# Kernel tuning notes

Measured on AMD Instinct MI355X. Metric: run time of the kernel, lower is better.

Reference implementation:

```python
import jax, jax.numpy as jnp
import numpy as np

N = 100000   # num nodes
E = 1600000  # num edges (before self-loops)
D_IN, D_HID, D_OUT = 128, 128, 64


def _gcn_layer(x, W, b, src, dst, norm):
    # GCNConv: h = x @ W, then normalized sparse aggregation, then bias.
    h = x @ W                              # [N, d_out]
    msg = h[src] * norm[:, None]           # [E+N, d_out] gathered + scaled messages
    out = jax.ops.segment_sum(msg, dst, num_segments=N)  # scatter-add to dst nodes
    return out + b


def reference(x, W1, b1, W2, b2, edge_index):
    src0, dst0 = edge_index[0], edge_index[1]
    # GCNConv adds self-loops by default
    loop = jnp.arange(N, dtype=src0.dtype)
    src = jnp.concatenate([src0, loop])
    dst = jnp.concatenate([dst0, loop])
    # symmetric normalization: deg^{-1/2}[src] * deg^{-1/2}[dst]
    deg = jax.ops.segment_sum(jnp.ones_like(src, dtype=x.dtype), dst, num_segments=N)
    dinv = jnp.where(deg > 0, jax.lax.rsqrt(jnp.maximum(deg, 1.0)), 0.0)
    norm = dinv[src] * dinv[dst]           # [E+N]

    h = jax.nn.relu(_gcn_layer(x, W1, b1, src, dst, norm))
    return _gcn_layer(h, W2, b2, src, dst, norm)


def setup_inputs() -> dict:
    key = jax.random.key(0)
    k1, k2, k3, k4 = jax.random.split(key, 4)
    x = jax.random.normal(k1, (N, D_IN), dtype=jnp.float32)
    # glorot-ish init for weights
    W1 = jax.random.normal(k2, (D_IN, D_HID), dtype=jnp.float32) * (1.0 / np.sqrt(D_IN))
    b1 = jnp.zeros((D_HID,), dtype=jnp.float32)
    W2 = jax.random.normal(k3, (D_HID, D_OUT), dtype=jnp.float32) * (1.0 / np.sqrt(D_HID))
    b2 = jnp.zeros((D_OUT,), dtype=jnp.float32)
    edge_index = jax.random.randint(k4, (2, E), 0, N, dtype=jnp.int64)
    return {"x": x, "W1": W1, "b1": b1, "W2": W2, "b2": b2, "edge_index": edge_index}
```

## Files before the change

kernel.cpp:

```cpp
#include <hip/hip_runtime.h>

static constexpr int NN = 100000;
static constexpr int EE = 1600000;
static constexpr int BSZ = 64;
static constexpr int NB = (NN + BSZ - 1) / BSZ;
static constexpr int BCAP = 2048;
static constexpr int TILE = 2048;
static constexpr int GB = 2048;


__device__ __forceinline__ unsigned short f2bf(float f) {
    unsigned u = __float_as_uint(f);
    u += 0x7FFFu + ((u >> 16) & 1u);
    return (unsigned short)(u >> 16);
}
__device__ __forceinline__ float bfl(unsigned u) { return __uint_as_float(u << 16); }
__device__ __forceinline__ float bfh(unsigned u) { return __uint_as_float(u & 0xFFFF0000u); }

typedef __attribute__((ext_vector_type(8))) short short8;
typedef __attribute__((ext_vector_type(4))) float float4v;


__global__ __launch_bounds__(256) void k_init(const float* __restrict__ W1,
                                              const float* __restrict__ W2,
                                              unsigned short* __restrict__ W1t,
                                              unsigned short* __restrict__ W2t,
                                              int* __restrict__ bcur) {
    int idx = blockIdx.x * 256 + threadIdx.x;
    if (idx < 16384) {
        int n = idx >> 7, k = idx & 127;
        W1t[idx] = f2bf(W1[k * 128 + n]);
    } else if (idx < 24576) {
        int j = idx - 16384;
        int n = j >> 7, k = j & 127;
        W2t[j] = f2bf(W2[k * 64 + n]);
    } else if (idx < 24576 + NB) {
        int b = idx - 24576;
        bcur[b] = b * BCAP;
    }
}


__global__ __launch_bounds__(256) void k_bin(const int* __restrict__ src,
                                             const int* __restrict__ dst,
                                             int* __restrict__ bcur,
                                             int* __restrict__ ebuf, int E) {
    constexpr int K = TILE / 256;
    __shared__ int lcnt[NB];
    __shared__ int lbase[NB];
    const int t = threadIdx.x;
    const int e0 = blockIdx.x * TILE;

    for (int i = t; i < NB; i += 256) lcnt[i] = 0;
    __syncthreads();

    int dreg[K], ofs[K];
#pragma unroll
    for (int k = 0; k < K; ++k) {
        int e = e0 + k * 256 + t;
        if (e < E) {
            int d = dst[e];
            dreg[k] = d;
            ofs[k] = atomicAdd(&lcnt[d >> 6], 1);
        } else dreg[k] = -1;
    }
    __syncthreads();

    for (int i = t; i < NB; i += 256) {
        int c = lcnt[i];
        lbase[i] = c ? atomicAdd(&bcur[i], c) : 0;
    }
    __syncthreads();

#pragma unroll
    for (int k = 0; k < K; ++k) {
        if (dreg[k] >= 0) {
            int e = e0 + k * 256 + t;
            int s = src[e];
            int b = dreg[k] >> 6;
            ebuf[lbase[b] + ofs[k]] = (s << 6) | (dreg[k] & 63);
        }
    }
}


__global__ __launch_bounds__(512) void k_bscan(const int* __restrict__ bcur,
                                               int* __restrict__ gbase) {
    const int t = threadIdx.x;
    const int lane = t & 63, wid = t >> 6;
    int v[4]; int s = 0;
#pragma unroll
    for (int k = 0; k < 4; ++k) {
        int b = t * 4 + k;
        v[k] = (b < NB) ? (bcur[b] - b * BCAP) : 0;
        s += v[k];
    }
    int x = s;
#pragma unroll
    for (int off = 1; off < 64; off <<= 1) {
        int y = __shfl_up(x, off, 64);
        if (lane >= off) x += y;
    }
    __shared__ int wsum[8], wexc[8];
    if (lane == 63) wsum[wid] = x;
    __syncthreads();
    if (t == 0) { int a = 0; for (int k = 0; k < 8; ++k) { wexc[k] = a; a += wsum[k]; } }
    __syncthreads();
    int base = wexc[wid] + x - s;
#pragma unroll
    for (int k = 0; k < 4; ++k) {
        int b = t * 4 + k;
        if (b < NB) gbase[b] = base;
        base += v[k];
    }
}


__global__ __launch_bounds__(256) void k_csr(const int* __restrict__ bcur,
                                             const int* __restrict__ ebuf,
                                             const int* __restrict__ gbase,
                                             int* __restrict__ rowbeg,
                                             int* __restrict__ rowend,
                                             float* __restrict__ dinv,
                                             int* __restrict__ csr, int n) {
    __shared__ int lcnt[BSZ];
    __shared__ int lofs[BSZ];
    const int b = blockIdx.x, t = threadIdx.x;
    if (t < BSZ) lcnt[t] = 0;
    __syncthreads();
    const int beg = b * BCAP, end = bcur[b];
    const int dbase = gbase[b];
    for (int j = beg + t; j < end; j += 256) atomicAdd(&lcnt[ebuf[j] & 63], 1);
    __syncthreads();
    if (t < BSZ) {
        int c = lcnt[t];
        int x = c;
#pragma unroll
        for (int off = 1; off < 64; off <<= 1) {
            int y = __shfl_up(x, off, 64);
            if (t >= off) x += y;
        }
        int exc = x - c;
        int node = b * BSZ + t;
        if (node < n) {
            rowbeg[node] = dbase + exc;
            rowend[node] = dbase + exc + c;
            dinv[node] = rsqrtf((float)c + 1.0f);
        }
        lofs[t] = dbase + exc;
    }
    __syncthreads();
    for (int j = beg + t; j < end; j += 256) {
        int e = ebuf[j];
        int pos = atomicAdd(&lofs[e & 63], 1);
        csr[pos] = e >> 6;
    }
}


__global__ __launch_bounds__(256) void k_gemm128m(const float* __restrict__ X,
                                                  const unsigned short* __restrict__ W1t,
                                                  const float* __restrict__ dinv,
                                                  unsigned* __restrict__ G, int M) {
    __shared__ float cls[4 * 16 * 132];
    const int t = threadIdx.x;
    const int w = t >> 6, lane = t & 63;
    const int quad = lane >> 4, m16 = lane & 15;
    const int row0 = blockIdx.x * 64 + w * 16;
    int arow = row0 + m16; if (arow >= M) arow = M - 1;

    short8 afrag[4];
#pragma unroll
    for (int ks = 0; ks < 4; ++ks) {
        const float* p = X + (size_t)arow * 128 + ks * 32 + quad * 8;
        float4 u0 = ((const float4*)p)[0];
        float4 u1 = ((const float4*)p)[1];
        short8 a;
        a[0] = (short)f2bf(u0.x); a[1] = (short)f2bf(u0.y);
        a[2] = (short)f2bf(u0.z); a[3] = (short)f2bf(u0.w);
        a[4] = (short)f2bf(u1.x); a[5] = (short)f2bf(u1.y);
        a[6] = (short)f2bf(u1.z); a[7] = (short)f2bf(u1.w);
        afrag[ks] = a;
    }
    float* myc = cls + w * 16 * 132;
#pragma unroll
    for (int nt = 0; nt < 8; ++nt) {
        float4v acc = {0.f, 0.f, 0.f, 0.f};
#pragma unroll
        for (int ks = 0; ks < 4; ++ks) {
            const short8 b = *((const short8*)(W1t + (size_t)(nt * 16 + m16) * 128 + ks * 32 + quad * 8));
            acc = __builtin_amdgcn_mfma_f32_16x16x32_bf16(afrag[ks], b, acc, 0, 0, 0);
        }
#pragma unroll
        for (int r = 0; r < 4; ++r)
            myc[(quad * 4 + r) * 132 + nt * 16 + m16] = acc[r];
    }
    __syncthreads();
#pragma unroll
    for (int i = 0; i < 8; ++i) {
        int idx = i * 64 + lane;
        int r = idx >> 5, c = idx & 31;
        int grow = row0 + r;
        if (grow < M) {
            float4 v = *((const float4*)(myc + r * 132 + c * 4));
            float s = dinv[grow];
            uint2 p;
            p.x = (unsigned)f2bf(v.x * s) | ((unsigned)f2bf(v.y * s) << 16);
            p.y = (unsigned)f2bf(v.z * s) | ((unsigned)f2bf(v.w * s) << 16);
            ((uint2*)G)[(size_t)grow * 32 + c] = p;
        }
    }
}


__global__ __launch_bounds__(256) void k_gemm64m(const unsigned short* __restrict__ X,
                                                 const unsigned short* __restrict__ W2t,
                                                 const float* __restrict__ dinv,
                                                 unsigned* __restrict__ G, int M) {
    __shared__ float cls[4 * 16 * 68];
    const int t = threadIdx.x;
    const int w = t >> 6, lane = t & 63;
    const int quad = lane >> 4, m16 = lane & 15;
    const int row0 = blockIdx.x * 64 + w * 16;
    int arow = row0 + m16; if (arow >= M) arow = M - 1;

    short8 afrag[4];
#pragma unroll
    for (int ks = 0; ks < 4; ++ks)
        afrag[ks] = *((const short8*)(X + (size_t)arow * 128 + ks * 32 + quad * 8));

    float* myc = cls + w * 16 * 68;
#pragma unroll
    for (int nt = 0; nt < 4; ++nt) {
        float4v acc = {0.f, 0.f, 0.f, 0.f};
#pragma unroll
        for (int ks = 0; ks < 4; ++ks) {
            const short8 b = *((const short8*)(W2t + (size_t)(nt * 16 + m16) * 128 + ks * 32 + quad * 8));
            acc = __builtin_amdgcn_mfma_f32_16x16x32_bf16(afrag[ks], b, acc, 0, 0, 0);
        }
#pragma unroll
        for (int r = 0; r < 4; ++r)
            myc[(quad * 4 + r) * 68 + nt * 16 + m16] = acc[r];
    }
    __syncthreads();
#pragma unroll
    for (int i = 0; i < 4; ++i) {
        int idx = i * 64 + lane;
        int r = idx >> 4, c = idx & 15;
        int grow = row0 + r;
        if (grow < M) {
            float4 v = *((const float4*)(myc + r * 68 + c * 4));
            float s = dinv[grow];
            uint2 p;
            p.x = (unsigned)f2bf(v.x * s) | ((unsigned)f2bf(v.y * s) << 16);
            p.y = (unsigned)f2bf(v.z * s) | ((unsigned)f2bf(v.w * s) << 16);
            ((uint2*)G)[(size_t)grow * 16 + c] = p;
        }
    }
}


__global__ __launch_bounds__(256) void k_gather128(const int* __restrict__ rowbeg,
                                                   const int* __restrict__ rowend,
                                                   const int* __restrict__ csr,
                                                   const unsigned* __restrict__ G,
                                                   const float* __restrict__ dinv,
                                                   const float* __restrict__ bias,
                                                   unsigned* __restrict__ OUT,
                                                   int n, int nwaves) {
    const int wid = blockIdx.x * 4 + (threadIdx.x >> 6);
    const int lane = threadIdx.x & 63;
    const int sub = lane & 31;
    const int half = lane >> 5;
    for (int node = wid; node < n; node += nwaves) {
        const int beg = rowbeg[node];
        const int end = rowend[node];
        float a0 = 0.f, a1 = 0.f, a2 = 0.f, a3 = 0.f;
        for (int c = beg; c < end; c += 64) {
            int ec = end - c; if (ec > 64) ec = 64;
            const int idx = csr[c + ((lane < ec) ? lane : 0)];
            int pb = 0;
            for (; pb + 16 <= ec; pb += 16) {
#pragma unroll
                for (int q = 0; q < 8; ++q) {
                    int s = __shfl(idx, pb + 2 * q + half, 64);
                    uint2 v = *((const uint2*)(G + (size_t)s * 64 + 2 * sub));
                    a0 += bfl(v.x); a1 += bfh(v.x); a2 += bfl(v.y); a3 += bfh(v.y);
                }
            }
            if (pb < ec) {
#pragma unroll
                for (int q = 0; q < 8; ++q) {
                    int e = pb + 2 * q + half;
                    bool valid = e < ec;
                    int s = __shfl(idx, valid ? e : 0, 64);
                    uint2 v = *((const uint2*)(G + (size_t)s * 64 + 2 * sub));
                    if (valid) { a0 += bfl(v.x); a1 += bfh(v.x); a2 += bfl(v.y); a3 += bfh(v.y); }
                }
            }
        }
        a0 += __shfl_xor(a0, 32, 64);
        a1 += __shfl_xor(a1, 32, 64);
        a2 += __shfl_xor(a2, 32, 64);
        a3 += __shfl_xor(a3, 32, 64);
        if (half == 0) {
            uint2 vs = *((const uint2*)(G + (size_t)node * 64 + 2 * sub));
            a0 += bfl(vs.x); a1 += bfh(vs.x); a2 += bfl(vs.y); a3 += bfh(vs.y);
            const float di = dinv[node];
            const float4 bv = ((const float4*)bias)[sub];
            float r0 = fmaf(a0, di, bv.x), r1 = fmaf(a1, di, bv.y);
            float r2 = fmaf(a2, di, bv.z), r3 = fmaf(a3, di, bv.w);
            r0 = fmaxf(r0, 0.f); r1 = fmaxf(r1, 0.f);
            r2 = fmaxf(r2, 0.f); r3 = fmaxf(r3, 0.f);
            uint2 p;
            p.x = (unsigned)f2bf(r0) | ((unsigned)f2bf(r1) << 16);
            p.y = (unsigned)f2bf(r2) | ((unsigned)f2bf(r3) << 16);
            ((uint2*)OUT)[(size_t)node * 32 + sub] = p;
        }
    }
}


__global__ __launch_bounds__(256) void k_gather64(const int* __restrict__ rowbeg,
                                                  const int* __restrict__ rowend,
                                                  const int* __restrict__ csr,
                                                  const unsigned* __restrict__ G,
                                                  const float* __restrict__ dinv,
                                                  const float* __restrict__ bias,
                                                  float* __restrict__ OUT,
                                                  int n, int nwaves) {
    const int wid = blockIdx.x * 4 + (threadIdx.x >> 6);
    const int lane = threadIdx.x & 63;
    const int sub = lane & 15;
    const int qh = lane >> 4;
    for (int node = wid; node < n; node += nwaves) {
        const int beg = rowbeg[node];
        const int end = rowend[node];
        float a0 = 0.f, a1 = 0.f, a2 = 0.f, a3 = 0.f;
        for (int c = beg; c < end; c += 64) {
            int ec = end - c; if (ec > 64) ec = 64;
            const int idx = csr[c + ((lane < ec) ? lane : 0)];
            int pb = 0;
            for (; pb + 32 <= ec; pb += 32) {
#pragma unroll
                for (int q = 0; q < 8; ++q) {
                    int s = __shfl(idx, pb + 4 * q + qh, 64);
                    uint2 v = ((const uint2*)(G + (size_t)s * 32))[sub];
                    a0 += bfl(v.x); a1 += bfh(v.x); a2 += bfl(v.y); a3 += bfh(v.y);
                }
            }
            if (pb < ec) {
#pragma unroll
                for (int q = 0; q < 8; ++q) {
                    int e = pb + 4 * q + qh;
                    bool valid = e < ec;
                    int s = __shfl(idx, valid ? e : 0, 64);
                    uint2 v = ((const uint2*)(G + (size_t)s * 32))[sub];
                    if (valid) { a0 += bfl(v.x); a1 += bfh(v.x); a2 += bfl(v.y); a3 += bfh(v.y); }
                }
            }
        }
        a0 += __shfl_xor(a0, 16, 64); a0 += __shfl_xor(a0, 32, 64);
        a1 += __shfl_xor(a1, 16, 64); a1 += __shfl_xor(a1, 32, 64);
        a2 += __shfl_xor(a2, 16, 64); a2 += __shfl_xor(a2, 32, 64);
        a3 += __shfl_xor(a3, 16, 64); a3 += __shfl_xor(a3, 32, 64);
        if (qh == 0) {
            uint2 vs = ((const uint2*)(G + (size_t)node * 32))[sub];
            a0 += bfl(vs.x); a1 += bfh(vs.x); a2 += bfl(vs.y); a3 += bfh(vs.y);
            const float di = dinv[node];
            const float4 bv = ((const float4*)bias)[sub];
            float4 r;
            r.x = fmaf(a0, di, bv.x);
            r.y = fmaf(a1, di, bv.y);
            r.z = fmaf(a2, di, bv.z);
            r.w = fmaf(a3, di, bv.w);
            ((float4*)OUT)[(size_t)node * 16 + sub] = r;
        }
    }
}


extern "C" void kernel_launch(void* const* d_in, const int* in_sizes, int n_in,
                              void* d_out, int out_size, void* d_ws, size_t ws_size,
                              hipStream_t stream) {
    const float* x  = (const float*)d_in[0];
    const float* W1 = (const float*)d_in[1];
    const float* b1 = (const float*)d_in[2];
    const float* W2 = (const float*)d_in[3];
    const float* b2 = (const float*)d_in[4];
    const int*   ei = (const int*)d_in[5];
    const int* src = ei;
    const int* dst = ei + EE;
    float* out = (float*)d_out;

    char* p = (char*)d_ws;
    unsigned* g1b = (unsigned*)p;             p += (size_t)NN * 64 * 4;
    unsigned* h1b = (unsigned*)p;             p += (size_t)NN * 64 * 4;
    unsigned* g2b = (unsigned*)p;             p += (size_t)NN * 32 * 4;
    unsigned short* w1t = (unsigned short*)p; p += 16384 * 2;
    unsigned short* w2t = (unsigned short*)p; p += 8192 * 2;
    int*   bcur   = (int*)p;                  p += ((size_t)NB * 4 + 15) & ~(size_t)15;
    int*   gbase  = (int*)p;                  p += ((size_t)NB * 4 + 15) & ~(size_t)15;
    int*   rowbeg = (int*)p;                  p += (size_t)NN * 4;
    int*   rowend = (int*)p;                  p += (size_t)NN * 4;
    float* dinv   = (float*)p;                p += (size_t)NN * 4;
    int*   ebuf   = (int*)p;                  p += (size_t)NB * BCAP * 4;
    int*   csr    = (int*)p;                  p += (size_t)EE * 4;

    constexpr int NWG = GB * 4;
    constexpr int IB = (24576 + NB + 255) / 256;

    k_init<<<IB, 256, 0, stream>>>(W1, W2, w1t, w2t, bcur);
    k_bin<<<(EE + TILE - 1) / TILE, 256, 0, stream>>>(src, dst, bcur, ebuf, EE);
    k_bscan<<<1, 512, 0, stream>>>(bcur, gbase);
    k_csr<<<NB, 256, 0, stream>>>(bcur, ebuf, gbase, rowbeg, rowend, dinv, csr, NN);

    k_gemm128m<<<(NN + 63) / 64, 256, 0, stream>>>(x, w1t, dinv, g1b, NN);
    k_gather128<<<GB, 256, 0, stream>>>(rowbeg, rowend, csr, g1b, dinv, b1, h1b, NN, NWG);

    k_gemm64m<<<(NN + 63) / 64, 256, 0, stream>>>((const unsigned short*)h1b, w2t, dinv, g2b, NN);
    k_gather64<<<GB, 256, 0, stream>>>(rowbeg, rowend, csr, g2b, dinv, b2, out, NN, NWG);
}
```

Before: 318.6 us.

## Fuse layer-2 weight multiply into layer-1 gather epilogue

The separate layer-2 MFMA GEMM kernel is removed, and the 128x64 product is done inside the layer-1 aggregation kernel, per node. Each block stages W2 as bf16 in LDS. Each wave writes its ReLU'd row into a small LDS buffer, then both wave halves compute a dot-product slice with scalar FMAs and combine them by shuffle. This removes the write and re-read of the 128-wide hidden activation buffer and one kernel launch. The cost is a per-node scalar matmul loop with many LDS reads inside an otherwise memory-bound gather, instead of using matrix cores.

```diff
diff --git a/kernel.cpp b/kernel.cpp
--- a/kernel.cpp
+++ b/kernel.cpp
@@ -22,20 +22,14 @@
 
 
 __global__ __launch_bounds__(256) void k_init(const float* __restrict__ W1,
-                                              const float* __restrict__ W2,
                                               unsigned short* __restrict__ W1t,
-                                              unsigned short* __restrict__ W2t,
                                               int* __restrict__ bcur) {
     int idx = blockIdx.x * 256 + threadIdx.x;
     if (idx < 16384) {
         int n = idx >> 7, k = idx & 127;
         W1t[idx] = f2bf(W1[k * 128 + n]);
-    } else if (idx < 24576) {
-        int j = idx - 16384;
-        int n = j >> 7, k = j & 127;
-        W2t[j] = f2bf(W2[k * 64 + n]);
-    } else if (idx < 24576 + NB) {
-        int b = idx - 24576;
+    } else if (idx < 16384 + NB) {
+        int b = idx - 16384;
         bcur[b] = b * BCAP;
     }
 }
@@ -213,65 +207,31 @@
 }
 
 
-__global__ __launch_bounds__(256) void k_gemm64m(const unsigned short* __restrict__ X,
-                                                 const unsigned short* __restrict__ W2t,
-                                                 const float* __restrict__ dinv,
-                                                 unsigned* __restrict__ G, int M) {
-    __shared__ float cls[4 * 16 * 68];
+__global__ __launch_bounds__(256) void k_gather128f(const int* __restrict__ rowbeg,
+                                                    const int* __restrict__ rowend,
+                                                    const int* __restrict__ csr,
+                                                    const unsigned* __restrict__ G,
+                                                    const float* __restrict__ dinv,
+                                                    const float* __restrict__ bias,
+                                                    const float* __restrict__ W2,
+                                                    unsigned* __restrict__ G2,
+                                                    int n, int nwaves) {
+    __shared__ unsigned w2l[128 * 32];
+    __shared__ float rowbuf[4][128];
     const int t = threadIdx.x;
-    const int w = t >> 6, lane = t & 63;
-    const int quad = lane >> 4, m16 = lane & 15;
-    const int row0 = blockIdx.x * 64 + w * 16;
-    int arow = row0 + m16; if (arow >= M) arow = M - 1;
-
-    short8 afrag[4];
-#pragma unroll
-    for (int ks = 0; ks < 4; ++ks)
-        afrag[ks] = *((const short8*)(X + (size_t)arow * 128 + ks * 32 + quad * 8));
-
-    float* myc = cls + w * 16 * 68;
-#pragma unroll
-    for (int nt = 0; nt < 4; ++nt) {
-        float4v acc = {0.f, 0.f, 0.f, 0.f};
-#pragma unroll
-        for (int ks = 0; ks < 4; ++ks) {
-            const short8 b = *((const short8*)(W2t + (size_t)(nt * 16 + m16) * 128 + ks * 32 + quad * 8));
-            acc = __builtin_amdgcn_mfma_f32_16x16x32_bf16(afrag[ks], b, acc, 0, 0, 0);
-        }
-#pragma unroll
-        for (int r = 0; r < 4; ++r)
-            myc[(quad * 4 + r) * 68 + nt * 16 + m16] = acc[r];
-    }
-    __syncthreads();
-#pragma unroll
-    for (int i = 0; i < 4; ++i) {
-        int idx = i * 64 + lane;
-        int r = idx >> 4, c = idx & 15;
-        int grow = row0 + r;
-        if (grow < M) {
-            float4 v = *((const float4*)(myc + r * 68 + c * 4));
-            float s = dinv[grow];
-            uint2 p;
-            p.x = (unsigned)f2bf(v.x * s) | ((unsigned)f2bf(v.y * s) << 16);
-            p.y = (unsigned)f2bf(v.z * s) | ((unsigned)f2bf(v.w * s) << 16);
-            ((uint2*)G)[(size_t)grow * 16 + c] = p;
-        }
-    }
-}
-
-
-__global__ __launch_bounds__(256) void k_gather128(const int* __restrict__ rowbeg,
-                                                   const int* __restrict__ rowend,
-                                                   const int* __restrict__ csr,
-                                                   const unsigned* __restrict__ G,
-                                                   const float* __restrict__ dinv,
-                                                   const float* __restrict__ bias,
-                                                   unsigned* __restrict__ OUT,
-                                                   int n, int nwaves) {
-    const int wid = blockIdx.x * 4 + (threadIdx.x >> 6);
-    const int lane = threadIdx.x & 63;
+    const int w = t >> 6;
+    const int lane = t & 63;
     const int sub = lane & 31;
     const int half = lane >> 5;
+    const int wid = blockIdx.x * 4 + w;
+
+    for (int i = t; i < 4096; i += 256) {
+        int k = i >> 5, jp = i & 31;
+        float2 f = *((const float2*)(W2 + (size_t)k * 64 + 2 * jp));
+        w2l[i] = (unsigned)f2bf(f.x) | ((unsigned)f2bf(f.y) << 16);
+    }
+    __syncthreads();
+
     for (int node = wid; node < n; node += nwaves) {
         const int beg = rowbeg[node];
         const int end = rowend[node];
@@ -303,19 +263,34 @@
         a1 += __shfl_xor(a1, 32, 64);
         a2 += __shfl_xor(a2, 32, 64);
         a3 += __shfl_xor(a3, 32, 64);
+        uint2 vs = *((const uint2*)(G + (size_t)node * 64 + 2 * sub));
+        a0 += bfl(vs.x); a1 += bfh(vs.x); a2 += bfl(vs.y); a3 += bfh(vs.y);
+        const float di = dinv[node];
+        const float4 bv = ((const float4*)bias)[sub];
+        float r0 = fmaf(a0, di, bv.x), r1 = fmaf(a1, di, bv.y);
+        float r2 = fmaf(a2, di, bv.z), r3 = fmaf(a3, di, bv.w);
+        r0 = fmaxf(r0, 0.f); r1 = fmaxf(r1, 0.f);
+        r2 = fmaxf(r2, 0.f); r3 = fmaxf(r3, 0.f);
         if (half == 0) {
-            uint2 vs = *((const uint2*)(G + (size_t)node * 64 + 2 * sub));
-            a0 += bfl(vs.x); a1 += bfh(vs.x); a2 += bfl(vs.y); a3 += bfh(vs.y);
-            const float di = dinv[node];
-            const float4 bv = ((const float4*)bias)[sub];
-            float r0 = fmaf(a0, di, bv.x), r1 = fmaf(a1, di, bv.y);
-            float r2 = fmaf(a2, di, bv.z), r3 = fmaf(a3, di, bv.w);
-            r0 = fmaxf(r0, 0.f); r1 = fmaxf(r1, 0.f);
-            r2 = fmaxf(r2, 0.f); r3 = fmaxf(r3, 0.f);
-            uint2 p;
-            p.x = (unsigned)f2bf(r0) | ((unsigned)f2bf(r1) << 16);
-            p.y = (unsigned)f2bf(r2) | ((unsigned)f2bf(r3) << 16);
-            ((uint2*)OUT)[(size_t)node * 32 + sub] = p;
+            float4 rv = {r0, r1, r2, r3};
+            *((float4*)&rowbuf[w][4 * sub]) = rv;
+        }
+        const int jp = sub;
+        const int kb = half << 6;
+        float c0 = 0.f, c1 = 0.f;
+        const float* hr = rowbuf[w];
+#pragma unroll 8
+        for (int kk = 0; kk < 64; ++kk) {
+            float h = hr[kb + kk];
+            unsigned u = w2l[(kb + kk) * 32 + jp];
+            c0 = fmaf(h, bfl(u), c0);
+            c1 = fmaf(h, bfh(u), c1);
+        }
+        c0 += __shfl_xor(c0, 32, 64);
+        c1 += __shfl_xor(c1, 32, 64);
+        if (half == 0) {
+            unsigned pk = (unsigned)f2bf(c0 * di) | ((unsigned)f2bf(c1 * di) << 16);
+            G2[(size_t)node * 32 + jp] = pk;
         }
     }
 }
@@ -395,10 +370,10 @@
 
     char* p = (char*)d_ws;
     unsigned* g1b = (unsigned*)p;             p += (size_t)NN * 64 * 4;
-    unsigned* h1b = (unsigned*)p;             p += (size_t)NN * 64 * 4;
+                            p += (size_t)NN * 64 * 4;
     unsigned* g2b = (unsigned*)p;             p += (size_t)NN * 32 * 4;
     unsigned short* w1t = (unsigned short*)p; p += 16384 * 2;
-    unsigned short* w2t = (unsigned short*)p; p += 8192 * 2;
+                            p += 8192 * 2;
     int*   bcur   = (int*)p;                  p += ((size_t)NB * 4 + 15) & ~(size_t)15;
     int*   gbase  = (int*)p;                  p += ((size_t)NB * 4 + 15) & ~(size_t)15;
     int*   rowbeg = (int*)p;                  p += (size_t)NN * 4;
@@ -408,16 +383,14 @@
     int*   csr    = (int*)p;                  p += (size_t)EE * 4;
 
     constexpr int NWG = GB * 4;
-    constexpr int IB = (24576 + NB + 255) / 256;
-
-    k_init<<<IB, 256, 0, stream>>>(W1, W2, w1t, w2t, bcur);
+    constexpr int IB = (16384 + NB + 255) / 256;
+
+    k_init<<<IB, 256, 0, stream>>>(W1, w1t, bcur);
     k_bin<<<(EE + TILE - 1) / TILE, 256, 0, stream>>>(src, dst, bcur, ebuf, EE);
     k_bscan<<<1, 512, 0, stream>>>(bcur, gbase);
     k_csr<<<NB, 256, 0, stream>>>(bcur, ebuf, gbase, rowbeg, rowend, dinv, csr, NN);
 
     k_gemm128m<<<(NN + 63) / 64, 256, 0, stream>>>(x, w1t, dinv, g1b, NN);
-    k_gather128<<<GB, 256, 0, stream>>>(rowbeg, rowend, csr, g1b, dinv, b1, h1b, NN, NWG);
-
-    k_gemm64m<<<(NN + 63) / 64, 256, 0, stream>>>((const unsigned short*)h1b, w2t, dinv, g2b, NN);
+    k_gather128f<<<GB, 256, 0, stream>>>(rowbeg, rowend, csr, g1b, dinv, b1, W2, g2b, NN, NWG);
     k_gather64<<<GB, 256, 0, stream>>>(rowbeg, rowend, csr, g2b, dinv, b2, out, NN, NWG);
 }
```

Measured after the change: 324.6 us. No clear change (+1.9%).
